# Performance work log

Measured on AMD Instinct MI355X. Metric: run time of the kernel, lower is better.

The kernel has to match this reference:

```python
import jax, jax.numpy as jnp
import numpy as np
from jax import lax

SIGMA = 1.5
KSIZE = 11  # int(6*1.5+1)=10 -> even -> 11
PAD = KSIZE // 2


def _gaussian_kernel_3d(ksize: int, sigma: float, dtype=jnp.float32):
    coords = jnp.arange(ksize, dtype=dtype) - (ksize // 2)
    g = jnp.exp(-(coords ** 2) / (2.0 * sigma ** 2))
    g = g / jnp.sum(g)
    # dense rank-1 separable outer product -> [k, k, k]
    k3 = g[:, None, None] * g[None, :, None] * g[None, None, :]
    return k3


def setup_inputs() -> dict:
    key = jax.random.key(0)
    x = jax.random.normal(key, (4, 1, 160, 192, 192), dtype=jnp.float32)
    return {"x": x}


def reference(x):
    # Faithful to torch: full dense 3D conv with the k^3 Gaussian kernel,
    # 'same' padding of kernel_size//2, single in/out channel.
    k3 = _gaussian_kernel_3d(KSIZE, SIGMA, x.dtype)
    w = k3[None, None]  # [O=1, I=1, kD, kH, kW]
    out = lax.conv_general_dilated(
        x, w,
        window_strides=(1, 1, 1),
        padding=[(PAD, PAD)] * 3,
        dimension_numbers=("NCDHW", "OIDHW", "NCDHW"),
    )
    return out
```

## Files before the change

### kernel.cpp

```cpp
#include <hip/hip_runtime.h>
#include <hip/hip_bf16.h>
#include <math.h>

#define KSIZE 11
#define PAD 5

struct GaussW { float w[KSIZE]; };

#define B_    4
#define D_    160
#define H_    192
#define W_    192
#define W4_   48

#define TW4    16
#define TH     48
#define DCH    10
#define NH     (H_ / TH)
#define NWT    (W_ / (TW4*4))
#define NDC    (D_ / DCH)
#define NBLK_A (B_ * NH * NWT * NDC)
#define INROWS (TH + 10)
#define INW4   (TW4 + 4)
#define IN_STR4 21
#define WT_STR4 17
#define NSTAGE (INROWS * INW4)
#define NWIT   (INROWS * 4)

static __device__ inline unsigned short f2bf(float f) {
    __hip_bfloat16 h = __float2bfloat16(f);
    return __builtin_bit_cast(unsigned short, h);
}

__global__ __launch_bounds__(256, 3) void blur_wh(const float4* __restrict__ src,
                                                  ushort4* __restrict__ wsb,
                                                  GaussW g) {
    __shared__ __align__(16) float lds_in[INROWS * IN_STR4 * 4];
    __shared__ __align__(16) float lds_wt[INROWS * WT_STR4 * 4];

    int bid = blockIdx.x;
    int L = (bid & 7) * (NBLK_A / 8) + (bid >> 3);
    int wx = L % NWT; L /= NWT;
    int hy = L % NH;  L /= NH;
    int dc = L % NDC;
    int b  = L / NDC;

    const int h0  = hy * TH;
    const int w0q = wx * TW4;
    const int d0  = dc * DCH;
    const int tid = threadIdx.x;

    float4 pf[5];
    auto issue = [&](int d) {
        const float4* plane = src + (b * D_ + d) * (H_ * W4_);
#pragma unroll
        for (int j = 0; j < 5; ++j) {
            pf[j] = make_float4(0.f, 0.f, 0.f, 0.f);
            int it = tid + j * 256;
            if (it < NSTAGE) {
                int ir = it / INW4, jc = it - ir * INW4;
                int h = h0 - PAD + ir;
                int q = w0q - 2 + jc;
                if (h >= 0 && h < H_ && q >= 0 && q < W4_)
                    pf[j] = plane[h * W4_ + q];
            }
        }
    };
    auto stage_write = [&]() {
#pragma unroll
        for (int j = 0; j < 5; ++j) {
            int it = tid + j * 256;
            if (it < NSTAGE) {
                int ir = it / INW4, jc = it - ir * INW4;
                *(float4*)&lds_in[(ir * IN_STR4 + jc) * 4] = pf[j];
            }
        }
    };

    issue(d0);
    stage_write();
    issue(d0 + 1);
    __syncthreads();

    for (int p = 0; p < DCH; ++p) {
        if (tid < NWIT) {
            const int gq = tid & 3, r = tid >> 2;
            float win[32];
            const float* row = &lds_in[(r * IN_STR4 + gq * 4) * 4];
#pragma unroll
            for (int u = 0; u < 8; ++u) {
                float4 v = *(const float4*)&row[u * 4];
                win[4*u+0] = v.x; win[4*u+1] = v.y;
                win[4*u+2] = v.z; win[4*u+3] = v.w;
            }
            float o[16];
#pragma unroll
            for (int i = 0; i < 16; ++i) {
                float a = 0.f;
#pragma unroll
                for (int t = 0; t < KSIZE; ++t) a += g.w[t] * win[i + 3 + t];
                o[i] = a;
            }
            float* wrow = &lds_wt[(r * WT_STR4 + gq * 4) * 4];
#pragma unroll
            for (int c = 0; c < 4; ++c)
                *(float4*)&wrow[c * 4] =
                    make_float4(o[4*c], o[4*c+1], o[4*c+2], o[4*c+3]);
        }
        __syncthreads();

        if (p + 1 < DCH) stage_write();
        if (p + 2 < DCH) issue(d0 + p + 2);

        {
            const int c4 = tid & 15, grp = tid >> 4;
            float4 a0 = make_float4(0.f,0.f,0.f,0.f);
            float4 a1 = a0, a2 = a0;
#pragma unroll
            for (int j = 0; j < 13; ++j) {
                float4 v = *(const float4*)&lds_wt[((3*grp + j) * WT_STR4 + c4) * 4];
                if (j <= 10) {
                    float wt = g.w[j];
                    a0.x += wt*v.x; a0.y += wt*v.y; a0.z += wt*v.z; a0.w += wt*v.w;
                }
                if (j >= 1 && j <= 11) {
                    float wt = g.w[j-1];
                    a1.x += wt*v.x; a1.y += wt*v.y; a1.z += wt*v.z; a1.w += wt*v.w;
                }
                if (j >= 2) {
                    float wt = g.w[j-2];
                    a2.x += wt*v.x; a2.y += wt*v.y; a2.z += wt*v.z; a2.w += wt*v.w;
                }
            }
            const int d = d0 + p;
            ushort4* wp = wsb + (b * D_ + d) * (H_ * W4_) + w0q + c4;
            wp[(h0 + 3*grp + 0) * W4_] = make_ushort4(f2bf(a0.x), f2bf(a0.y), f2bf(a0.z), f2bf(a0.w));
            wp[(h0 + 3*grp + 1) * W4_] = make_ushort4(f2bf(a1.x), f2bf(a1.y), f2bf(a1.z), f2bf(a1.w));
            wp[(h0 + 3*grp + 2) * W4_] = make_ushort4(f2bf(a2.x), f2bf(a2.y), f2bf(a2.z), f2bf(a2.w));
        }
        __syncthreads();
    }
}

static __device__ inline float4 bf4_to_f4(ushort4 u) {
    return make_float4(__uint_as_float((unsigned)u.x << 16),
                       __uint_as_float((unsigned)u.y << 16),
                       __uint_as_float((unsigned)u.z << 16),
                       __uint_as_float((unsigned)u.w << 16));
}

template <int STR4, int LEN, int CH>
__global__ __launch_bounds__(256) void blur_d_slide(const ushort4* __restrict__ src,
                                                    float4* __restrict__ dst,
                                                    GaussW g, int ncol) {
    int tid = blockIdx.x * blockDim.x + threadIdx.x;
    int col = tid % ncol;
    int chunk = tid / ncol;
    int c0 = chunk * CH;
    int inner = col % STR4;
    int outer = col / STR4;
    int base = outer * (LEN * STR4) + inner;

    float4 ring[KSIZE];
#pragma unroll
    for (int j = 0; j < KSIZE - 1; ++j) {
        int cc = c0 - PAD + j;
        float4 v = make_float4(0.f, 0.f, 0.f, 0.f);
        if (cc >= 0 && cc < LEN) v = bf4_to_f4(src[base + cc * STR4]);
        ring[j] = v;
    }
#pragma unroll
    for (int k = 0; k < CH; ++k) {
        int cc = c0 + k + PAD;
        float4 v = make_float4(0.f, 0.f, 0.f, 0.f);
        if (cc < LEN) v = bf4_to_f4(src[base + cc * STR4]);
        ring[(KSIZE - 1 + k) % KSIZE] = v;

        float4 acc = make_float4(0.f, 0.f, 0.f, 0.f);
#pragma unroll
        for (int t = 0; t < KSIZE; ++t) {
            float4 u = ring[(k + t) % KSIZE];
            float wt = g.w[t];
            acc.x += wt * u.x; acc.y += wt * u.y;
            acc.z += wt * u.z; acc.w += wt * u.w;
        }
        dst[base + (c0 + k) * STR4] = acc;
    }
}

__global__ void blur_dense_fallback(const float* __restrict__ src,
                                    float* __restrict__ dst,
                                    GaussW g, int B, int D, int H, int W) {
    long n = (long)B * D * H * W;
    long i = (long)blockIdx.x * blockDim.x + threadIdx.x;
    if (i >= n) return;
    int w = (int)(i % W);
    long r = i / W;
    int h = (int)(r % H); r /= H;
    int d = (int)(r % D);
    int b = (int)(r / D);

    float acc = 0.f;
    for (int td = 0; td < KSIZE; ++td) {
        int dd = d + td - PAD;
        if (dd < 0 || dd >= D) continue;
        for (int th = 0; th < KSIZE; ++th) {
            int hh = h + th - PAD;
            if (hh < 0 || hh >= H) continue;
            float wdh = g.w[td] * g.w[th];
            const float* row = src + (((long)b * D + dd) * H + hh) * W;
            for (int tw = 0; tw < KSIZE; ++tw) {
                int ww = w + tw - PAD;
                if (ww < 0 || ww >= W) continue;
                acc += wdh * g.w[tw] * row[ww];
            }
        }
    }
    dst[i] = acc;
}

extern "C" void kernel_launch(void* const* d_in, const int* in_sizes, int n_in,
                              void* d_out, int out_size, void* d_ws, size_t ws_size,
                              hipStream_t stream) {
    const float* x = (const float*)d_in[0];
    float* out = (float*)d_out;
    (void)in_sizes; (void)n_in; (void)out_size;

    const long n = (long)B_ * D_ * H_ * W_;

    GaussW g;
    {
        double tmp[KSIZE], s = 0.0;
        for (int i = 0; i < KSIZE; ++i) {
            double dd = (double)(i - PAD);
            tmp[i] = exp(-(dd * dd) / (2.0 * 1.5 * 1.5));
            s += tmp[i];
        }
        for (int i = 0; i < KSIZE; ++i) g.w[i] = (float)(tmp[i] / s);
    }

    if (ws_size >= (size_t)n * sizeof(unsigned short)) {
        blur_wh<<<NBLK_A, 256, 0, stream>>>((const float4*)x, (ushort4*)d_ws, g);
        const int ncol = B_ * H_ * W4_;
        const int threads = ncol * (D_ / 32);
        blur_d_slide<9216, 160, 32><<<threads / 256, 256, 0, stream>>>(
            (const ushort4*)d_ws, (float4*)out, g, ncol);
    } else {
        long gridN = (n + 255) / 256;
        blur_dense_fallback<<<(int)gridN, 256, 0, stream>>>(x, out, g, B_, D_, H_, W_);
    }
}
```

Measured before the change: 63.99 us.

## Load W-conv windows directly from global into registers, double-buffer row LDS

Drops the LDS staging of raw input tiles. Each thread now loads its 8 float4 window directly from global memory into registers, with precomputed clamped offsets and multiplicative masks for the borders. The W-filtered results alternate between two LDS buffers, so one barrier per depth plane is enough and the next plane's loads overlap the current compute. The cost is redundant global reads of overlapping windows (8 float4 per 4 outputs) and more register pressure, now that the occupancy hint of 3 in launch_bounds is removed.

New measurement: 73.04 us. +14.1%, slower.

```diff
diff --git a/kernel.cpp b/kernel.cpp
--- a/kernel.cpp
+++ b/kernel.cpp
@@ -21,22 +21,20 @@
 #define NDC    (D_ / DCH)
 #define NBLK_A (B_ * NH * NWT * NDC)
 #define INROWS (TH + 10)
-#define INW4   (TW4 + 4)
-#define IN_STR4 21
 #define WT_STR4 17
-#define NSTAGE (INROWS * INW4)
 #define NWIT   (INROWS * 4)
+#define PSTR4  (H_ * W4_)
 
 static __device__ inline unsigned short f2bf(float f) {
     __hip_bfloat16 h = __float2bfloat16(f);
     return __builtin_bit_cast(unsigned short, h);
 }
 
-__global__ __launch_bounds__(256, 3) void blur_wh(const float4* __restrict__ src,
-                                                  ushort4* __restrict__ wsb,
-                                                  GaussW g) {
-    __shared__ __align__(16) float lds_in[INROWS * IN_STR4 * 4];
-    __shared__ __align__(16) float lds_wt[INROWS * WT_STR4 * 4];
+__global__ __launch_bounds__(256) void blur_wh2(const float4* __restrict__ src,
+                                                ushort4* __restrict__ wsb,
+                                                GaussW g) {
+    __shared__ __align__(16) float wtA[INROWS * WT_STR4 * 4];
+    __shared__ __align__(16) float wtB[INROWS * WT_STR4 * 4];
 
     int bid = blockIdx.x;
     int L = (bid & 7) * (NBLK_A / 8) + (bid >> 3);
@@ -50,48 +48,50 @@
     const int d0  = dc * DCH;
     const int tid = threadIdx.x;
 
-    float4 pf[5];
-    auto issue = [&](int d) {
-        const float4* plane = src + (b * D_ + d) * (H_ * W4_);
-#pragma unroll
-        for (int j = 0; j < 5; ++j) {
-            pf[j] = make_float4(0.f, 0.f, 0.f, 0.f);
-            int it = tid + j * 256;
-            if (it < NSTAGE) {
-                int ir = it / INW4, jc = it - ir * INW4;
-                int h = h0 - PAD + ir;
-                int q = w0q - 2 + jc;
-                if (h >= 0 && h < H_ && q >= 0 && q < W4_)
-                    pf[j] = plane[h * W4_ + q];
+    const int wr   = tid >> 2;
+    const int wq   = (tid & 3) * 4;
+    const bool wact = (wr < INROWS);
+    const int h_in = h0 - PAD + wr;
+    const int q0   = w0q + wq - 2;
+    const int hc   = min(max(h_in, 0), H_ - 1);
+    const bool vh  = (h_in >= 0) && (h_in < H_);
+    int   off4[8];
+    float fm[8];
+#pragma unroll
+    for (int u = 0; u < 8; ++u) {
+        int q = q0 + u;
+        bool vq = (q >= 0) && (q < W4_);
+        off4[u] = hc * W4_ + min(max(q, 0), W4_ - 1);
+        fm[u] = (vh && vq) ? 1.f : 0.f;
+    }
+
+    const int c4  = tid & 15;
+    const int grp = tid >> 4;
+
+    const float4* pin = src + (b * D_ + d0) * PSTR4;
+    ushort4* pout = wsb + (b * D_ + d0) * PSTR4 + (h0 + 3 * grp) * W4_ + w0q + c4;
+
+    float4 winA[8], winB[8];
+
+    auto load_win = [&](float4 (&win)[8], const float4* p) {
+        if (wact) {
+#pragma unroll
+            for (int u = 0; u < 8; ++u) {
+                float4 v = p[off4[u]];
+                float m = fm[u];
+                win[u].x = v.x * m; win[u].y = v.y * m;
+                win[u].z = v.z * m; win[u].w = v.w * m;
             }
         }
     };
-    auto stage_write = [&]() {
-#pragma unroll
-        for (int j = 0; j < 5; ++j) {
-            int it = tid + j * 256;
-            if (it < NSTAGE) {
-                int ir = it / INW4, jc = it - ir * INW4;
-                *(float4*)&lds_in[(ir * IN_STR4 + jc) * 4] = pf[j];
-            }
-        }
-    };
-
-    issue(d0);
-    stage_write();
-    issue(d0 + 1);
-    __syncthreads();
-
-    for (int p = 0; p < DCH; ++p) {
-        if (tid < NWIT) {
-            const int gq = tid & 3, r = tid >> 2;
+
+    auto wconv = [&](const float4 (&win8)[8], float* wt) {
+        if (wact) {
             float win[32];
-            const float* row = &lds_in[(r * IN_STR4 + gq * 4) * 4];
 #pragma unroll
             for (int u = 0; u < 8; ++u) {
-                float4 v = *(const float4*)&row[u * 4];
-                win[4*u+0] = v.x; win[4*u+1] = v.y;
-                win[4*u+2] = v.z; win[4*u+3] = v.w;
+                win[4*u+0] = win8[u].x; win[4*u+1] = win8[u].y;
+                win[4*u+2] = win8[u].z; win[4*u+3] = win8[u].w;
             }
             float o[16];
 #pragma unroll
@@ -101,44 +101,51 @@
                 for (int t = 0; t < KSIZE; ++t) a += g.w[t] * win[i + 3 + t];
                 o[i] = a;
             }
-            float* wrow = &lds_wt[(r * WT_STR4 + gq * 4) * 4];
+            float* wrow = &wt[(wr * WT_STR4 + wq) * 4];
 #pragma unroll
             for (int c = 0; c < 4; ++c)
                 *(float4*)&wrow[c * 4] =
                     make_float4(o[4*c], o[4*c+1], o[4*c+2], o[4*c+3]);
         }
+    };
+
+    auto hconv = [&](const float* wt, ushort4* op) {
+        float4 a0 = make_float4(0.f,0.f,0.f,0.f);
+        float4 a1 = a0, a2 = a0;
+#pragma unroll
+        for (int j = 0; j < 13; ++j) {
+            float4 v = *(const float4*)&wt[((3*grp + j) * WT_STR4 + c4) * 4];
+            if (j <= 10) {
+                float wt_ = g.w[j];
+                a0.x += wt_*v.x; a0.y += wt_*v.y; a0.z += wt_*v.z; a0.w += wt_*v.w;
+            }
+            if (j >= 1 && j <= 11) {
+                float wt_ = g.w[j-1];
+                a1.x += wt_*v.x; a1.y += wt_*v.y; a1.z += wt_*v.z; a1.w += wt_*v.w;
+            }
+            if (j >= 2) {
+                float wt_ = g.w[j-2];
+                a2.x += wt_*v.x; a2.y += wt_*v.y; a2.z += wt_*v.z; a2.w += wt_*v.w;
+            }
+        }
+        op[0        ] = make_ushort4(f2bf(a0.x), f2bf(a0.y), f2bf(a0.z), f2bf(a0.w));
+        op[W4_      ] = make_ushort4(f2bf(a1.x), f2bf(a1.y), f2bf(a1.z), f2bf(a1.w));
+        op[2 * W4_  ] = make_ushort4(f2bf(a2.x), f2bf(a2.y), f2bf(a2.z), f2bf(a2.w));
+    };
+
+    load_win(winA, pin);
+    pin += PSTR4;
+
+    for (int p = 0; p < DCH; p += 2) {
+        load_win(winB, pin); pin += PSTR4;
+        wconv(winA, wtA);
         __syncthreads();
-
-        if (p + 1 < DCH) stage_write();
-        if (p + 2 < DCH) issue(d0 + p + 2);
-
-        {
-            const int c4 = tid & 15, grp = tid >> 4;
-            float4 a0 = make_float4(0.f,0.f,0.f,0.f);
-            float4 a1 = a0, a2 = a0;
-#pragma unroll
-            for (int j = 0; j < 13; ++j) {
-                float4 v = *(const float4*)&lds_wt[((3*grp + j) * WT_STR4 + c4) * 4];
-                if (j <= 10) {
-                    float wt = g.w[j];
-                    a0.x += wt*v.x; a0.y += wt*v.y; a0.z += wt*v.z; a0.w += wt*v.w;
-                }
-                if (j >= 1 && j <= 11) {
-                    float wt = g.w[j-1];
-                    a1.x += wt*v.x; a1.y += wt*v.y; a1.z += wt*v.z; a1.w += wt*v.w;
-                }
-                if (j >= 2) {
-                    float wt = g.w[j-2];
-                    a2.x += wt*v.x; a2.y += wt*v.y; a2.z += wt*v.z; a2.w += wt*v.w;
-                }
-            }
-            const int d = d0 + p;
-            ushort4* wp = wsb + (b * D_ + d) * (H_ * W4_) + w0q + c4;
-            wp[(h0 + 3*grp + 0) * W4_] = make_ushort4(f2bf(a0.x), f2bf(a0.y), f2bf(a0.z), f2bf(a0.w));
-            wp[(h0 + 3*grp + 1) * W4_] = make_ushort4(f2bf(a1.x), f2bf(a1.y), f2bf(a1.z), f2bf(a1.w));
-            wp[(h0 + 3*grp + 2) * W4_] = make_ushort4(f2bf(a2.x), f2bf(a2.y), f2bf(a2.z), f2bf(a2.w));
-        }
+        hconv(wtA, pout); pout += PSTR4;
+        if (p + 2 < DCH) { load_win(winA, pin); }
+        pin += PSTR4;
+        wconv(winB, wtB);
         __syncthreads();
+        hconv(wtB, pout); pout += PSTR4;
     }
 }
 
@@ -240,7 +247,7 @@
     }
 
     if (ws_size >= (size_t)n * sizeof(unsigned short)) {
-        blur_wh<<<NBLK_A, 256, 0, stream>>>((const float4*)x, (ushort4*)d_ws, g);
+        blur_wh2<<<NBLK_A, 256, 0, stream>>>((const float4*)x, (ushort4*)d_ws, g);
         const int ncol = B_ * H_ * W4_;
         const int threads = ncol * (D_ / 32);
         blur_d_slide<9216, 160, 32><<<threads / 256, 256, 0, stream>>>(
```
